# Optimization experiments

Measured on AMD Instinct MI355X. Metric: run time of the kernel, lower is better.

The kernel has to match this reference:

```python
import jax, jax.numpy as jnp
import numpy as np

E = 1024
H = 16
D = E // H
FF = 4096
EPS = 1e-5


def _layernorm(x, gamma, beta):
    mu = jnp.mean(x, axis=-1, keepdims=True)
    var = jnp.var(x, axis=-1, keepdims=True)
    return (x - mu) * jax.lax.rsqrt(var + EPS) * gamma + beta


def setup_inputs() -> dict:
    key = jax.random.key(0)
    ks = jax.random.split(key, 12)
    B, C = 4, 2048
    s_e = 1.0 / np.sqrt(E)
    s_f = 1.0 / np.sqrt(FF)
    return {
        "x": jax.random.normal(ks[0], (B, C, E), dtype=jnp.float32),
        "ln1_g": jnp.ones((E,), jnp.float32),
        "ln1_b": jnp.zeros((E,), jnp.float32),
        "Wq": jax.random.normal(ks[1], (E, H * D), jnp.float32) * s_e,
        "Wk": jax.random.normal(ks[2], (E, H * D), jnp.float32) * s_e,
        "Wv": jax.random.normal(ks[3], (E, H * D), jnp.float32) * s_e,
        "Wo": jax.random.normal(ks[4], (H * D, E), jnp.float32) * s_e,
        "ln2_g": jnp.ones((E,), jnp.float32),
        "ln2_b": jnp.zeros((E,), jnp.float32),
        "W1": jax.random.normal(ks[5], (E, FF), jnp.float32) * s_e,
        "b1": jnp.zeros((FF,), jnp.float32),
        "W2": jax.random.normal(ks[6], (FF, E), jnp.float32) * s_f,
        "b2": jnp.zeros((E,), jnp.float32),
    }


def reference(x, ln1_g, ln1_b, Wq, Wk, Wv, Wo, ln2_g, ln2_b, W1, b1, W2, b2):
    B, C, _ = x.shape

    # --- pre-LN causal self-attention ---
    h = _layernorm(x, ln1_g, ln1_b)
    Q = (h @ Wq).reshape(B, C, H, D).transpose(0, 2, 1, 3)  # [B,H,C,D]
    K = (h @ Wk).reshape(B, C, H, D).transpose(0, 2, 1, 3)
    V = (h @ Wv).reshape(B, C, H, D).transpose(0, 2, 1, 3)

    scores = jnp.einsum("bhqd,bhkd->bhqk", Q, K) / jnp.sqrt(jnp.float32(D))
    causal = jnp.tril(jnp.ones((C, C), dtype=bool))
    scores = jnp.where(causal, scores, -jnp.inf)
    weights = jax.nn.softmax(scores, axis=-1)  # dropout omitted (eval)
    hidden = jnp.einsum("bhqk,bhkd->bhqd", weights, V)
    hidden = hidden.transpose(0, 2, 1, 3).reshape(B, C, H * D)
    x = x + hidden @ Wo

    # --- FFN ---
    h2 = _layernorm(x, ln2_g, ln2_b)
    h2 = jax.nn.gelu(h2 @ W1 + b1, approximate=False)
    x = x + (h2 @ W2 + b2)
    return x
```

## Files before the change

kernel.cpp:

```cpp
#include <hip/hip_runtime.h>

typedef __bf16 bf16x8 __attribute__((ext_vector_type(8)));
typedef float f32x4 __attribute__((ext_vector_type(4)));
typedef unsigned short u16x8 __attribute__((ext_vector_type(8)));
typedef unsigned short u16x4 __attribute__((ext_vector_type(4)));

__device__ __forceinline__ unsigned short f2bf(float f) {
    return __builtin_bit_cast(unsigned short, (__bf16)f);
}
__device__ __forceinline__ float bf2f(unsigned short u) {
    return (float)__builtin_bit_cast(__bf16, u);
}

__device__ __forceinline__ float fexp2(float x) {
#if __has_builtin(__builtin_amdgcn_exp2f)
    return __builtin_amdgcn_exp2f(x);
#else
    float r; asm("v_exp_f32 %0, %1\n\ts_nop 1" : "=v"(r) : "v"(x)); return r;
#endif
}

__device__ __forceinline__ void gload_lds16(const unsigned short* g, unsigned short* l) {
    __builtin_amdgcn_global_load_lds(
        (const __attribute__((address_space(1))) unsigned int*)g,
        (__attribute__((address_space(3))) unsigned int*)l, 16, 0, 0);
}

#define VMW(n) asm volatile("s_waitcnt vmcnt(" #n ")" ::: "memory")
#define SBAR() __builtin_amdgcn_s_barrier()
#define SCHED0() __builtin_amdgcn_sched_barrier(0)

#define QSCALE 0.18033688011112042f

__global__ __launch_bounds__(256) void ln_kernel(
    const float* __restrict__ x, const float* __restrict__ g,
    const float* __restrict__ b, unsigned short* __restrict__ out)
{
    const int row = blockIdx.x;
    const int tid = threadIdx.x;
    const float4 v = reinterpret_cast<const float4*>(x + (size_t)row * 1024)[tid];
    float s = v.x + v.y + v.z + v.w;
    float q = v.x * v.x + v.y * v.y + v.z * v.z + v.w * v.w;
#pragma unroll
    for (int off = 32; off >= 1; off >>= 1) {
        s += __shfl_xor(s, off);
        q += __shfl_xor(q, off);
    }
    __shared__ float ss[4], sq[4];
    const int wid = tid >> 6, lane = tid & 63;
    if (lane == 0) { ss[wid] = s; sq[wid] = q; }
    __syncthreads();
    s = ss[0] + ss[1] + ss[2] + ss[3];
    q = sq[0] + sq[1] + sq[2] + sq[3];
    const float mu = s * (1.0f / 1024.0f);
    const float var = q * (1.0f / 1024.0f) - mu * mu;
    const float rs = rsqrtf(var + 1e-5f);
    const float4 gv = reinterpret_cast<const float4*>(g)[tid];
    const float4 bv = reinterpret_cast<const float4*>(b)[tid];
    u16x4 o;
    o[0] = f2bf((v.x - mu) * rs * gv.x + bv.x);
    o[1] = f2bf((v.y - mu) * rs * gv.y + bv.y);
    o[2] = f2bf((v.z - mu) * rs * gv.z + bv.z);
    o[3] = f2bf((v.w - mu) * rs * gv.w + bv.w);
    reinterpret_cast<u16x4*>(out + (size_t)row * 1024)[tid] = o;
}

__global__ __launch_bounds__(256) void convT_kernel(
    const float* __restrict__ W, unsigned short* __restrict__ Wt, int K, int N)
{
    __shared__ float t[32][33];
    const int n0 = blockIdx.x * 32, k0 = blockIdx.y * 32;
    const int tx = threadIdx.x & 31;
    const int ty = threadIdx.x >> 5;
#pragma unroll
    for (int i = 0; i < 4; i++)
        t[ty + 8 * i][tx] = W[(size_t)(k0 + ty + 8 * i) * N + (n0 + tx)];
    __syncthreads();
#pragma unroll
    for (int i = 0; i < 4; i++)
        Wt[(size_t)(n0 + ty + 8 * i) * K + (k0 + tx)] = f2bf(t[tx][ty + 8 * i]);
}

__global__ __launch_bounds__(256) void convT4_kernel(
    const float* __restrict__ A0, const float* __restrict__ A1,
    const float* __restrict__ A2, const float* __restrict__ A3,
    unsigned short* __restrict__ Wt)
{
    constexpr int E = 1024;
    const int z = blockIdx.z;
    const float* W = (z == 0) ? A0 : (z == 1) ? A1 : (z == 2) ? A2 : A3;
    unsigned short* dst = Wt + (size_t)z * E * E;
    __shared__ float t[32][33];
    const int n0 = blockIdx.x * 32, k0 = blockIdx.y * 32;
    const int tx = threadIdx.x & 31;
    const int ty = threadIdx.x >> 5;
#pragma unroll
    for (int i = 0; i < 4; i++)
        t[ty + 8 * i][tx] = W[(size_t)(k0 + ty + 8 * i) * E + (n0 + tx)];
    __syncthreads();
#pragma unroll
    for (int i = 0; i < 4; i++)
        dst[(size_t)(n0 + ty + 8 * i) * E + (k0 + tx)] = f2bf(t[tx][ty + 8 * i]);
}

__global__ __launch_bounds__(256) void gemm128_kernel(
    const unsigned short* __restrict__ A, const unsigned short* __restrict__ Bt,
    const float* __restrict__ resid, float* __restrict__ out, int M, int N, int K)
{
    __shared__ unsigned short Al[128][64];
    __shared__ unsigned short Bl[128][64];
    const int tid = threadIdx.x;
    const int lane = tid & 63, wid = tid >> 6;
    const int wr = wid >> 1, wc = wid & 1;
    const int li = lane & 15, lg = lane >> 4;
    const int m0 = blockIdx.y * 128, n0 = blockIdx.x * 128;
    const int srow = lane >> 3;
    const int schunk = ((lane & 7) ^ srow) * 8;
    const unsigned short* Asrc = A + (size_t)(m0 + wid * 32 + srow) * K + schunk;
    const unsigned short* Bsrc = Bt + (size_t)(n0 + wid * 32 + srow) * K + schunk;
    f32x4 acc[4][4] = {};

    for (int k0 = 0; k0 < K; k0 += 64) {
        __syncthreads();
#pragma unroll
        for (int i = 0; i < 4; i++) {
            gload_lds16(Asrc + k0 + (size_t)i * 8 * K, &Al[wid * 32 + i * 8][0]);
            gload_lds16(Bsrc + k0 + (size_t)i * 8 * K, &Bl[wid * 32 + i * 8][0]);
        }
        __syncthreads();
#pragma unroll
        for (int ks = 0; ks < 2; ks++) {
            bf16x8 af[4], bfr[4];
#pragma unroll
            for (int m = 0; m < 4; m++)
                af[m] = *reinterpret_cast<const bf16x8*>(
                    &Al[wr * 64 + m * 16 + li][((ks * 4 + lg) ^ (li & 7)) * 8]);
#pragma unroll
            for (int n = 0; n < 4; n++)
                bfr[n] = *reinterpret_cast<const bf16x8*>(
                    &Bl[wc * 64 + n * 16 + li][((ks * 4 + lg) ^ (li & 7)) * 8]);
#pragma unroll
            for (int m = 0; m < 4; m++)
#pragma unroll
                for (int n = 0; n < 4; n++)
                    acc[m][n] = __builtin_amdgcn_mfma_f32_16x16x32_bf16(af[m], bfr[n], acc[m][n], 0, 0, 0);
        }
    }

#pragma unroll
    for (int m = 0; m < 4; m++)
#pragma unroll
        for (int r = 0; r < 4; r++) {
            const int row = m0 + wr * 64 + m * 16 + lg * 4 + r;
#pragma unroll
            for (int n = 0; n < 4; n++) {
                const int col = n0 + wc * 64 + n * 16 + li;
                out[(size_t)row * N + col] = acc[m][n][r] + resid[(size_t)row * N + col];
            }
        }
}

#define DEFINE_GEMM256(NAME, EPI, SPLITK, MM, NN, KK)                                        \
__global__ __launch_bounds__(512, 2) void NAME(                                              \
    const unsigned short* __restrict__ A, const unsigned short* __restrict__ Bt,             \
    const float* __restrict__ bias, void* __restrict__ out)                                  \
{                                                                                            \
    constexpr int M = MM, N = NN, K = KK;                                                    \
    constexpr int GRID = SPLITK * (M >> 8) * (N >> 8);                                       \
    constexpr int nblk = (M >> 8) * (N >> 8);                                                \
    constexpr int cpx = GRID >> 3;                                                           \
    constexpr int nx = N >> 8;                                                               \
    constexpr int kLen = (SPLITK == 2) ? (K >> 1) : K;                                       \
    constexpr int NI = kLen >> 7;                                                            \
    __shared__ __align__(16) unsigned short Al[2][256][64];                                  \
    __shared__ __align__(16) unsigned short Bl[2][256][64];                                  \
    const int tid = threadIdx.x;                                                             \
    const int lane = tid & 63, wid = tid >> 6;                                               \
    const int wr = wid >> 2, wc = wid & 3;                                                   \
    const int li = lane & 15, lg = lane >> 4;                                                \
    const int swz = ((int)blockIdx.x & 7) * cpx + ((int)blockIdx.x >> 3);                    \
    int tsw = swz, sid = 0;                                                                  \
    if (SPLITK == 2) { sid = (swz >= nblk) ? 1 : 0; tsw = swz - sid * nblk; }                \
    const int bx = tsw % nx, by = tsw / nx;                                                  \
    const int m0 = by * 256, n0 = bx * 256;                                                  \
    const int kOff = (SPLITK == 2) ? sid * (K >> 1) : 0;                                     \
    const int srow = lane >> 3;                                                              \
    const int sgc = ((lane & 7) ^ srow) * 8;                                                 \
    const unsigned short* aSrc = A + (size_t)(m0 + wid * 16 + srow) * K + kOff + sgc;        \
    const unsigned short* bSrc = Bt + (size_t)(n0 + wid * 16 + srow) * K + kOff + sgc;       \
    unsigned short* aDst = &Al[0][wid * 16][0];                                              \
    unsigned short* bDst = &Bl[0][wid * 16][0];                                              \
    auto stA = [&](int u, int h) {                                                           \
        const unsigned short* s = aSrc + (size_t)(h * 128) * K + u * 64;                     \
        unsigned short* d = aDst + (u & 1) * (256 * 64) + h * 128 * 64;                      \
        gload_lds16(s, d);                                                                   \
        gload_lds16(s + (size_t)8 * K, d + 8 * 64);                                          \
    };                                                                                       \
    auto stB = [&](int u, int h) {                                                           \
        const unsigned short* s = bSrc + (size_t)(h * 128) * K + u * 64;                     \
        unsigned short* d = bDst + (u & 1) * (256 * 64) + h * 128 * 64;                      \
        gload_lds16(s, d);                                                                   \
        gload_lds16(s + (size_t)8 * K, d + 8 * 64);                                          \
    };                                                                                       \
    f32x4 acc[8][4] = {};                                                                    \
    bf16x8 af[8], bn0[4], bn1[4];                                                            \
    auto ldA = [&](int buf, int mh) {                                                        \
        _Pragma("unroll")                                                                    \
        for (int m = 0; m < 4; m++)                                                          \
            _Pragma("unroll")                                                                \
            for (int ks = 0; ks < 2; ks++)                                                   \
                af[m * 2 + ks] = *reinterpret_cast<const bf16x8*>(                           \
                    &Al[buf][wr * 128 + mh * 64 + m * 16 + li][((ks * 4 + lg) ^ (li & 7)) * 8]); \
    };                                                                                       \
    auto ldB = [&](bf16x8* dst, int buf, int nh) {                                           \
        _Pragma("unroll")                                                                    \
        for (int n = 0; n < 2; n++)                                                          \
            _Pragma("unroll")                                                                \
            for (int ks = 0; ks < 2; ks++)                                                   \
                dst[n * 2 + ks] = *reinterpret_cast<const bf16x8*>(                          \
                    &Bl[buf][wc * 64 + nh * 32 + n * 16 + li][((ks * 4 + lg) ^ (li & 7)) * 8]); \
    };                                                                                       \
    auto quad = [&](const bf16x8* bfr, int mh, int nh) {                                     \
        __builtin_amdgcn_s_setprio(1);                                                       \
        _Pragma("unroll")                                                                    \
        for (int ks = 0; ks < 2; ks++)                                                       \
            _Pragma("unroll")                                                                \
            for (int m = 0; m < 4; m++)                                                      \
                _Pragma("unroll")                                                            \
                for (int n = 0; n < 2; n++)                                                  \
                    acc[mh * 4 + m][nh * 2 + n] = __builtin_amdgcn_mfma_f32_16x16x32_bf16(   \
                        af[m * 2 + ks], bfr[n * 2 + ks], acc[mh * 4 + m][nh * 2 + n], 0, 0, 0); \
        __builtin_amdgcn_s_setprio(0);                                                       \
    };                                                                                       \
    stA(0, 0); stA(0, 1); stB(0, 0); stB(0, 1);                                              \
    stB(1, 0); stB(1, 1);                                                                    \
    VMW(4);                                                                                  \
    SBAR(); SCHED0();                                                                        \
    for (int I = 0; I < NI; ++I) {                                                           \
        const int u0 = 2 * I;                                                                \
        const bool hn = (I + 1 < NI);                                                        \
        ldA(0, 0); ldB(bn0, 0, 0);                                                           \
        stA(u0 + 1, 0);                                                                      \
        SBAR(); SCHED0();                                                                    \
        quad(bn0, 0, 0);                                                                     \
        SBAR(); SCHED0();                                                                    \
        ldB(bn1, 0, 1);                                                                      \
        stA(u0 + 1, 1);                                                                      \
        SBAR(); SCHED0();                                                                    \
        quad(bn1, 0, 1);                                                                     \
        SBAR(); SCHED0();                                                                    \
        ldA(0, 1);                                                                           \
        if (hn) stB(u0 + 2, 0);                                                              \
        SBAR(); SCHED0();                                                                    \
        quad(bn1, 1, 1);                                                                     \
        SBAR(); SCHED0();                                                                    \
        if (hn) stB(u0 + 2, 1);                                                              \
        SBAR(); SCHED0();                                                                    \
        quad(bn0, 1, 0);                                                                     \
        if (hn) { VMW(4); } else { VMW(0); }                                                 \
        SBAR(); SCHED0();                                                                    \
        ldA(1, 0); ldB(bn0, 1, 0);                                                           \
        if (hn) stA(u0 + 2, 0);                                                              \
        SBAR(); SCHED0();                                                                    \
        quad(bn0, 0, 0);                                                                     \
        SBAR(); SCHED0();                                                                    \
        ldB(bn1, 1, 1);                                                                      \
        if (hn) stA(u0 + 2, 1);                                                              \
        SBAR(); SCHED0();                                                                    \
        quad(bn1, 0, 1);                                                                     \
        SBAR(); SCHED0();                                                                    \
        ldA(1, 1);                                                                           \
        if (hn) stB(u0 + 3, 0);                                                              \
        SBAR(); SCHED0();                                                                    \
        quad(bn1, 1, 1);                                                                     \
        SBAR(); SCHED0();                                                                    \
        if (hn) stB(u0 + 3, 1);                                                              \
        SBAR(); SCHED0();                                                                    \
        quad(bn0, 1, 0);                                                                     \
        if (hn) { VMW(4); } else { VMW(0); }                                                 \
        SBAR(); SCHED0();                                                                    \
    }                                                                                        \
    _Pragma("unroll")                                                                        \
    for (int ma = 0; ma < 8; ma++) {                                                         \
        _Pragma("unroll")                                                                    \
        for (int r = 0; r < 4; r++) {                                                        \
            const int row = m0 + wr * 128 + ma * 16 + lg * 4 + r;                            \
            _Pragma("unroll")                                                                \
            for (int n = 0; n < 4; n++) {                                                    \
                const int col = n0 + wc * 64 + n * 16 + li;                                  \
                float v = acc[ma][n][r];                                                     \
                if constexpr (EPI == 2) {                                                    \
                    v += bias[col];                                                          \
                    float a2 = 1.5957691216f * (v + 0.044715f * v * v * v);                  \
                    a2 = fminf(a2, 80.0f);                                                   \
                    const float t = __expf(a2);                                              \
                    v = v * t * __builtin_amdgcn_rcpf(t + 1.0f);                             \
                    reinterpret_cast<unsigned short*>(out)[(size_t)row * N + col] = f2bf(v); \
                } else if constexpr (EPI == 4) {                                             \
                    unsigned short* op = reinterpret_cast<unsigned short*>(out) + (size_t)sid * M * N; \
                    op[(size_t)row * N + col] = f2bf(v);                                     \
                } else {                                                                     \
                    const float sc = (col < 1024) ? QSCALE : 1.0f;                           \
                    reinterpret_cast<unsigned short*>(out)[(size_t)row * N + col] = f2bf(v * sc); \
                }                                                                            \
            }                                                                                \
        }                                                                                    \
    }                                                                                        \
}

DEFINE_GEMM256(gemm_qkv, 5, 1, 8192, 3072, 1024)
DEFINE_GEMM256(gemm_w1,  2, 1, 8192, 4096, 1024)
DEFINE_GEMM256(gemm_w2,  4, 2, 8192, 1024, 4096)

__global__ __launch_bounds__(256) void w2red_kernel(
    const unsigned short* __restrict__ p0, const unsigned short* __restrict__ p1,
    const float* __restrict__ x1, const float* __restrict__ b2,
    float* __restrict__ out)
{
    const int i = blockIdx.x * 256 + threadIdx.x;
    const u16x8 a = reinterpret_cast<const u16x8*>(p0)[i];
    const u16x8 b = reinterpret_cast<const u16x8*>(p1)[i];
    const float4 r0 = reinterpret_cast<const float4*>(x1)[2 * i];
    const float4 r1 = reinterpret_cast<const float4*>(x1)[2 * i + 1];
    const int cb = (i & 127) * 8;
    const float4 bb0 = *reinterpret_cast<const float4*>(b2 + cb);
    const float4 bb1 = *reinterpret_cast<const float4*>(b2 + cb + 4);
    float4 o0, o1;
    o0.x = bf2f(a[0]) + bf2f(b[0]) + r0.x + bb0.x;
    o0.y = bf2f(a[1]) + bf2f(b[1]) + r0.y + bb0.y;
    o0.z = bf2f(a[2]) + bf2f(b[2]) + r0.z + bb0.z;
    o0.w = bf2f(a[3]) + bf2f(b[3]) + r0.w + bb0.w;
    o1.x = bf2f(a[4]) + bf2f(b[4]) + r1.x + bb1.x;
    o1.y = bf2f(a[5]) + bf2f(b[5]) + r1.y + bb1.y;
    o1.z = bf2f(a[6]) + bf2f(b[6]) + r1.z + bb1.z;
    o1.w = bf2f(a[7]) + bf2f(b[7]) + r1.w + bb1.w;
    reinterpret_cast<float4*>(out)[2 * i] = o0;
    reinterpret_cast<float4*>(out)[2 * i + 1] = o1;
}

__global__ __launch_bounds__(256, 4) void flash_kernel(
    const unsigned short* __restrict__ QKV, unsigned short* __restrict__ O)
{
    constexpr int C = 2048, HD3 = 3072, HD = 1024, NT = 32;
    __shared__ unsigned short Kl[2][64][64];
    __shared__ unsigned short Vt[2][64][64];
    __shared__ unsigned short Pl[64][64];
    const int tid = threadIdx.x;
    const int lane = tid & 63, wid = tid >> 6;
    const int li = lane & 15, lg = lane >> 4;
    const int flat = blockIdx.x;
    const int bh = flat & 63;
    const int pair = flat >> 6;
    const int b = bh >> 4, h = bh & 15;
    const size_t baseQ = ((size_t)b * C) * HD3 + (size_t)h * 64;
    const size_t baseK = baseQ + 1024;
    const size_t baseV = baseQ + 2048;
    const size_t baseO = ((size_t)b * C) * HD + (size_t)h * 64;

    const int srow = lane >> 3;
    const int sgc = ((lane & 7) ^ srow) * 8;
    const int vx = lane & 7;

    const u16x8 onesu = {0x3F80, 0x3F80, 0x3F80, 0x3F80, 0x3F80, 0x3F80, 0x3F80, 0x3F80};
    const bf16x8 ones = __builtin_bit_cast(bf16x8, onesu);

    for (int half = 0; half < 2; half++) {
        const int qt = (half == 0) ? pair : (NT - 1 - pair);
        const int q0 = qt * 64;
        const int qrow = q0 + wid * 16 + li;
        const bf16x8 qa0 = *reinterpret_cast<const bf16x8*>(&QKV[baseQ + (size_t)qrow * HD3 + lg * 8]);
        const bf16x8 qa1 = *reinterpret_cast<const bf16x8*>(&QKV[baseQ + (size_t)qrow * HD3 + 32 + lg * 8]);
        const int myrow0 = q0 + wid * 16 + lg * 4;

        f32x4 acc[4] = {};
        f32x4 accl = {};
        int cur = 0;

        auto stage = [&](int k0s, int buf) {
#pragma unroll
            for (int i = 0; i < 2; i++)
                gload_lds16(&QKV[baseK + (size_t)(k0s + wid * 16 + i * 8 + srow) * HD3 + sgc],
                            &Kl[buf][wid * 16 + i * 8][0]);
#pragma unroll
            for (int i = 0; i < 2; i++) {
                const int lkey = 8 * wid + srow + 32 * i;
                const u16x8 vv = *reinterpret_cast<const u16x8*>(
                    &QKV[baseV + (size_t)(k0s + lkey) * HD3 + vx * 8]);
                const int vc = wid + 4 * i;
#pragma unroll
                for (int j = 0; j < 8; j++)
                    Vt[buf][vx * 8 + j][((vc ^ j ^ vx) & 7) * 8 + srow] = vv[j];
            }
        };

        __syncthreads();
        stage(0, 0);
        __syncthreads();

        auto tile_body = [&](int t, bool diag, bool pre) {
            const int k0 = t * 64;
            u16x8 vr0, vr1;
            if (pre) {
                const int kn = k0 + 64;
#pragma unroll
                for (int i = 0; i < 2; i++)
                    gload_lds16(&QKV[baseK + (size_t)(kn + wid * 16 + i * 8 + srow) * HD3 + sgc],
                                &Kl[cur ^ 1][wid * 16 + i * 8][0]);
                vr0 = *reinterpret_cast<const u16x8*>(
                    &QKV[baseV + (size_t)(kn + 8 * wid + srow) * HD3 + vx * 8]);
                vr1 = *reinterpret_cast<const u16x8*>(
                    &QKV[baseV + (size_t)(kn + 8 * wid + srow + 32) * HD3 + vx * 8]);
            }

            f32x4 s[4] = {};
            __builtin_amdgcn_s_setprio(1);
#pragma unroll
            for (int n = 0; n < 4; n++) {
                const int row = n * 16 + li;
                const bf16x8 kb0 = *reinterpret_cast<const bf16x8*>(
                    &Kl[cur][row][(lg ^ (li & 7)) * 8]);
                const bf16x8 kb1 = *reinterpret_cast<const bf16x8*>(
                    &Kl[cur][row][((4 + lg) ^ (li & 7)) * 8]);
                s[n] = __builtin_amdgcn_mfma_f32_16x16x32_bf16(qa0, kb0, s[n], 0, 0, 0);
                s[n] = __builtin_amdgcn_mfma_f32_16x16x32_bf16(qa1, kb1, s[n], 0, 0, 0);
            }
            __builtin_amdgcn_s_setprio(0);

#pragma unroll
            for (int n = 0; n < 4; n++) {
#pragma unroll
                for (int r = 0; r < 4; r++) {
                    float pv = fexp2(s[n][r]);
                    if (diag) {
                        const int key = k0 + n * 16 + li;
                        if (key > myrow0 + r) pv = 0.0f;
                    }
                    Pl[wid * 16 + lg * 4 + r][((2 * n + (li >> 3) + 2 * lg) & 7) * 8 + (li & 7)] = f2bf(pv);
                }
            }

            if (pre) {
#pragma unroll
                for (int j = 0; j < 8; j++)
                    Vt[cur ^ 1][vx * 8 + j][((wid ^ j ^ vx) & 7) * 8 + srow] = vr0[j];
#pragma unroll
                for (int j = 0; j < 8; j++)
                    Vt[cur ^ 1][vx * 8 + j][(((wid + 4) ^ j ^ vx) & 7) * 8 + srow] = vr1[j];
            }

            __builtin_amdgcn_s_setprio(1);
#pragma unroll
            for (int ks = 0; ks < 2; ks++) {
                const bf16x8 pa = *reinterpret_cast<const bf16x8*>(
                    &Pl[wid * 16 + li][((ks * 4 + lg + 2 * (li >> 2)) & 7) * 8]);
#pragma unroll
                for (int n = 0; n < 4; n++) {
                    const int row = n * 16 + li;
                    const bf16x8 vb = *reinterpret_cast<const bf16x8*>(
                        &Vt[cur][row][(((ks * 4 + lg) ^ (row & 7) ^ (row >> 3)) & 7) * 8]);
                    acc[n] = __builtin_amdgcn_mfma_f32_16x16x32_bf16(pa, vb, acc[n], 0, 0, 0);
                }
                accl = __builtin_amdgcn_mfma_f32_16x16x32_bf16(pa, ones, accl, 0, 0, 0);
            }
            __builtin_amdgcn_s_setprio(0);

            __syncthreads();
            cur ^= 1;
        };

        for (int t = 0; t < qt; t++) tile_body(t, false, true);
        tile_body(qt, true, false);

#pragma unroll
        for (int r = 0; r < 4; r++) {
            const float inv = 1.0f / accl[r];
            const int row = myrow0 + r;
#pragma unroll
            for (int n = 0; n < 4; n++)
                O[baseO + (size_t)row * HD + n * 16 + li] = f2bf(acc[n][r] * inv);
        }
    }
}

extern "C" void kernel_launch(void* const* d_in, const int* in_sizes, int n_in,
                              void* d_out, int out_size, void* d_ws, size_t ws_size,
                              hipStream_t stream) {
    constexpr int B = 4, C = 2048, E = 1024, H = 16, FF = 4096;
    constexpr int M = B * C;

    const float* x     = (const float*)d_in[0];
    const float* ln1_g = (const float*)d_in[1];
    const float* ln1_b = (const float*)d_in[2];
    const float* Wq    = (const float*)d_in[3];
    const float* Wk    = (const float*)d_in[4];
    const float* Wv    = (const float*)d_in[5];
    const float* Wo    = (const float*)d_in[6];
    const float* ln2_g = (const float*)d_in[7];
    const float* ln2_b = (const float*)d_in[8];
    const float* W1    = (const float*)d_in[9];
    const float* b1    = (const float*)d_in[10];
    const float* W2    = (const float*)d_in[11];
    const float* b2    = (const float*)d_in[12];

    char* p = (char*)d_ws;
    auto alloc = [&](size_t bytes) { void* r = (void*)p; p += (bytes + 255) & ~(size_t)255; return r; };
    unsigned short* WqT  = (unsigned short*)alloc((size_t)E * E * 2);
    unsigned short* WkT  = (unsigned short*)alloc((size_t)E * E * 2);
    unsigned short* WvT  = (unsigned short*)alloc((size_t)E * E * 2);
    unsigned short* WoT  = (unsigned short*)alloc((size_t)E * E * 2);
    unsigned short* W1T  = (unsigned short*)alloc((size_t)E * FF * 2);
    unsigned short* W2T  = (unsigned short*)alloc((size_t)FF * E * 2);
    unsigned short* hb   = (unsigned short*)alloc((size_t)M * E * 2);
    unsigned short* QKVb = (unsigned short*)alloc((size_t)M * 3 * E * 2);
    unsigned short* attn = (unsigned short*)alloc((size_t)M * E * 2);
    float*          x1   = (float*)alloc((size_t)M * E * 4);
    unsigned short* h2   = (unsigned short*)alloc((size_t)M * E * 2);
    unsigned short* ff   = (unsigned short*)alloc((size_t)M * FF * 2);
    (void)WkT; (void)WvT;
    unsigned short* parts = hb;

    convT4_kernel<<<dim3(E / 32, E / 32, 4), 256, 0, stream>>>(Wq, Wk, Wv, Wo, WqT);
    convT_kernel<<<dim3(FF / 32, E / 32), 256, 0, stream>>>(W1, W1T, E, FF);
    convT_kernel<<<dim3(E / 32, FF / 32), 256, 0, stream>>>(W2, W2T, FF, E);

    ln_kernel<<<M, 256, 0, stream>>>(x, ln1_g, ln1_b, hb);

    gemm_qkv<<<dim3(384), 512, 0, stream>>>(hb, WqT, nullptr, QKVb);

    flash_kernel<<<dim3(1024), 256, 0, stream>>>(QKVb, attn);

    gemm128_kernel<<<dim3(E / 128, M / 128), 256, 0, stream>>>(
        attn, WoT, x, x1, M, E, E);

    ln_kernel<<<M, 256, 0, stream>>>(x1, ln2_g, ln2_b, h2);

    gemm_w1<<<dim3(512), 512, 0, stream>>>(h2, W1T, b1, ff);

    gemm_w2<<<dim3(256), 512, 0, stream>>>(ff, W2T, nullptr, parts);
    w2red_kernel<<<dim3(M * E / 8 / 256), 256, 0, stream>>>(
        parts, parts + (size_t)M * E, x1, b2, (float*)d_out);
}
```

Baseline: 352.0 us.

## Use 128-row query tiles with 8 waves sharing each K/V tile in flash attention

The flash attention kernel moves from 64-query tiles on 4 waves to 128-query tiles on 8 waves per block, so each staged 64-key K/V tile is reused by twice as many query rows. The grid is halved, each wave stages one 8-row slice of K and V instead of two, and the last two key tiles are treated as diagonal. The P-tile LDS swizzle is also changed. The aim is to halve K/V global loads and staging work per query row, at the cost of fewer blocks, more masked work on the diagonal tiles and heavier register pressure under the new launch bounds.

```diff
diff --git a/kernel.cpp b/kernel.cpp
--- a/kernel.cpp
+++ b/kernel.cpp
@@ -338,13 +338,13 @@
     reinterpret_cast<float4*>(out)[2 * i + 1] = o1;
 }
 
-__global__ __launch_bounds__(256, 4) void flash_kernel(
+__global__ __launch_bounds__(512, 6) void flash_kernel(
     const unsigned short* __restrict__ QKV, unsigned short* __restrict__ O)
 {
-    constexpr int C = 2048, HD3 = 3072, HD = 1024, NT = 32;
+    constexpr int C = 2048, HD3 = 3072, HD = 1024;
     __shared__ unsigned short Kl[2][64][64];
     __shared__ unsigned short Vt[2][64][64];
-    __shared__ unsigned short Pl[64][64];
+    __shared__ unsigned short Pl[128][64];
     const int tid = threadIdx.x;
     const int lane = tid & 63, wid = tid >> 6;
     const int li = lane & 15, lg = lane >> 4;
@@ -365,8 +365,8 @@
     const bf16x8 ones = __builtin_bit_cast(bf16x8, onesu);
 
     for (int half = 0; half < 2; half++) {
-        const int qt = (half == 0) ? pair : (NT - 1 - pair);
-        const int q0 = qt * 64;
+        const int qt = (half == 0) ? pair : (15 - pair);
+        const int q0 = qt * 128;
         const int qrow = q0 + wid * 16 + li;
         const bf16x8 qa0 = *reinterpret_cast<const bf16x8*>(&QKV[baseQ + (size_t)qrow * HD3 + lg * 8]);
         const bf16x8 qa1 = *reinterpret_cast<const bf16x8*>(&QKV[baseQ + (size_t)qrow * HD3 + 32 + lg * 8]);
@@ -375,22 +375,16 @@
         f32x4 acc[4] = {};
         f32x4 accl = {};
         int cur = 0;
+        const int nt = 2 * qt + 2;
 
         auto stage = [&](int k0s, int buf) {
-#pragma unroll
-            for (int i = 0; i < 2; i++)
-                gload_lds16(&QKV[baseK + (size_t)(k0s + wid * 16 + i * 8 + srow) * HD3 + sgc],
-                            &Kl[buf][wid * 16 + i * 8][0]);
-#pragma unroll
-            for (int i = 0; i < 2; i++) {
-                const int lkey = 8 * wid + srow + 32 * i;
-                const u16x8 vv = *reinterpret_cast<const u16x8*>(
-                    &QKV[baseV + (size_t)(k0s + lkey) * HD3 + vx * 8]);
-                const int vc = wid + 4 * i;
-#pragma unroll
-                for (int j = 0; j < 8; j++)
-                    Vt[buf][vx * 8 + j][((vc ^ j ^ vx) & 7) * 8 + srow] = vv[j];
-            }
+            gload_lds16(&QKV[baseK + (size_t)(k0s + wid * 8 + srow) * HD3 + sgc],
+                        &Kl[buf][wid * 8][0]);
+            const u16x8 vv = *reinterpret_cast<const u16x8*>(
+                &QKV[baseV + (size_t)(k0s + wid * 8 + srow) * HD3 + vx * 8]);
+#pragma unroll
+            for (int j = 0; j < 8; j++)
+                Vt[buf][vx * 8 + j][((wid ^ j ^ vx) & 7) * 8 + srow] = vv[j];
         };
 
         __syncthreads();
@@ -399,17 +393,13 @@
 
         auto tile_body = [&](int t, bool diag, bool pre) {
             const int k0 = t * 64;
-            u16x8 vr0, vr1;
+            u16x8 vr;
             if (pre) {
                 const int kn = k0 + 64;
-#pragma unroll
-                for (int i = 0; i < 2; i++)
-                    gload_lds16(&QKV[baseK + (size_t)(kn + wid * 16 + i * 8 + srow) * HD3 + sgc],
-                                &Kl[cur ^ 1][wid * 16 + i * 8][0]);
-                vr0 = *reinterpret_cast<const u16x8*>(
-                    &QKV[baseV + (size_t)(kn + 8 * wid + srow) * HD3 + vx * 8]);
-                vr1 = *reinterpret_cast<const u16x8*>(
-                    &QKV[baseV + (size_t)(kn + 8 * wid + srow + 32) * HD3 + vx * 8]);
+                gload_lds16(&QKV[baseK + (size_t)(kn + wid * 8 + srow) * HD3 + sgc],
+                            &Kl[cur ^ 1][wid * 8][0]);
+                vr = *reinterpret_cast<const u16x8*>(
+                    &QKV[baseV + (size_t)(kn + wid * 8 + srow) * HD3 + vx * 8]);
             }
 
             f32x4 s[4] = {};
@@ -435,24 +425,22 @@
                         const int key = k0 + n * 16 + li;
                         if (key > myrow0 + r) pv = 0.0f;
                     }
-                    Pl[wid * 16 + lg * 4 + r][((2 * n + (li >> 3) + 2 * lg) & 7) * 8 + (li & 7)] = f2bf(pv);
+                    Pl[wid * 16 + lg * 4 + r]
+                      [((2 * n + (li >> 3) + lg * 4 + r) & 7) * 8 + (li & 7)] = f2bf(pv);
                 }
             }
 
             if (pre) {
 #pragma unroll
                 for (int j = 0; j < 8; j++)
-                    Vt[cur ^ 1][vx * 8 + j][((wid ^ j ^ vx) & 7) * 8 + srow] = vr0[j];
-#pragma unroll
-                for (int j = 0; j < 8; j++)
-                    Vt[cur ^ 1][vx * 8 + j][(((wid + 4) ^ j ^ vx) & 7) * 8 + srow] = vr1[j];
+                    Vt[cur ^ 1][vx * 8 + j][((wid ^ j ^ vx) & 7) * 8 + srow] = vr[j];
             }
 
             __builtin_amdgcn_s_setprio(1);
 #pragma unroll
             for (int ks = 0; ks < 2; ks++) {
                 const bf16x8 pa = *reinterpret_cast<const bf16x8*>(
-                    &Pl[wid * 16 + li][((ks * 4 + lg + 2 * (li >> 2)) & 7) * 8]);
+                    &Pl[wid * 16 + li][((ks * 4 + lg + li) & 7) * 8]);
 #pragma unroll
                 for (int n = 0; n < 4; n++) {
                     const int row = n * 16 + li;
@@ -468,8 +456,7 @@
             cur ^= 1;
         };
 
-        for (int t = 0; t < qt; t++) tile_body(t, false, true);
-        tile_body(qt, true, false);
+        for (int t = 0; t < nt; t++) tile_body(t, t >= nt - 2, t < nt - 1);
 
 #pragma unroll
         for (int r = 0; r < 4; r++) {
@@ -527,7 +514,7 @@
 
     gemm_qkv<<<dim3(384), 512, 0, stream>>>(hb, WqT, nullptr, QKVb);
 
-    flash_kernel<<<dim3(1024), 256, 0, stream>>>(QKVb, attn);
+    flash_kernel<<<dim3(512), 512, 0, stream>>>(QKVb, attn);
 
     gemm128_kernel<<<dim3(E / 128, M / 128), 256, 0, stream>>>(
         attn, WoT, x, x1, M, E, E);
```

Measured after the change: 445.8 us. +26.6%, slower.
